# Performance work log

Hardware: AMD Instinct MI355X
Metric: run time of the kernel (lower is better)

The kernel has to match this reference:

```python
import jax, jax.numpy as jnp
import numpy as np

NU, NI, G, D, HD, OD = 8000, 10000, 4096, 64, 64, 64
ALPHA = 0.8      # self vs neighbor mixing in NodeApplyModule
EPS = 1e-8       # cosine-similarity denominator epsilon
NEG_BIG = -1e38  # replacement for all -inf rows


def setup_inputs() -> dict:
    key = jax.random.key(0)
    ks = jax.random.split(key, 24)
    def lin(k, o, i):
        return (jax.random.normal(k, (o, i), jnp.float32) * 0.02)
    def bias(k, o):
        return (jax.random.normal(k, (o,), jnp.float32) * 0.02)
    inp = {}
    inp["H"] = jax.random.randint(ks[0], (NU + NI, G), 0, 2, jnp.int32)
    inp["feats_weight"] = jax.random.normal(ks[1], (NU + NI, D), jnp.float32) * 0.1
    inp["num_groups"] = G
    # user SelfAttention params
    inp["u_Wq"] = lin(ks[2], HD, D); inp["u_bq"] = bias(ks[3], HD)
    inp["u_Wk"] = lin(ks[4], HD, D); inp["u_bk"] = bias(ks[5], HD)
    inp["u_Wv"] = lin(ks[6], HD, D); inp["u_bv"] = bias(ks[7], HD)
    inp["u_Ws"] = lin(ks[8], 1, NU); inp["u_bs"] = bias(ks[9], 1)
    # item SelfAttention params
    inp["i_Wq"] = lin(ks[10], HD, D); inp["i_bq"] = bias(ks[11], HD)
    inp["i_Wk"] = lin(ks[12], HD, D); inp["i_bk"] = bias(ks[13], HD)
    inp["i_Wv"] = lin(ks[14], HD, D); inp["i_bv"] = bias(ks[15], HD)
    inp["i_Ws"] = lin(ks[16], 1, NI); inp["i_bs"] = bias(ks[17], 1)
    # WeightedGCN NodeApplyModule linear: in_feats = 2*HD -> out_feats = OD
    inp["g_W"] = lin(ks[18], OD, 2 * HD); inp["g_b"] = bias(ks[19], OD)
    return inp


def _self_attention(x, mask, num_groups, Wq, bq, Wk, bk, Wv, bv, Ws, bs):
    # x: [N, D] ; mask: [N, G]
    q = x @ Wq.T + bq            # [N, HD]
    k = x @ Wk.T + bk            # [N, HD]
    v = x @ Wv.T + bv            # [N, HD]
    s = (q @ k.T) @ Ws.T + bs    # [N, 1]  (Linear(num_elem,1) over q@k.T)
    scores = jnp.broadcast_to(s.reshape(1, -1), (num_groups, x.shape[0]))  # [G, N]
    maskT = (mask == 0).T        # [G, N]
    scores = jnp.where(maskT, -jnp.inf, scores)
    all_inf = jnp.all(scores == -jnp.inf, axis=1, keepdims=True)
    scores = jnp.where(all_inf, jnp.float32(NEG_BIG), scores)
    w = jax.nn.softmax(scores, axis=1)   # [G, N]
    return w @ v, w                      # [G, HD], [G, N]


def reference(H, feats_weight, num_groups,
              u_Wq, u_bq, u_Wk, u_bk, u_Wv, u_bv, u_Ws, u_bs,
              i_Wq, i_bq, i_Wk, i_bk, i_Wv, i_bv, i_Ws, i_bs,
              g_W, g_b):
    users_feats = feats_weight[:NU]
    items_feats = feats_weight[NU:]
    users_mask = H[:NU]
    items_mask = H[NU:]

    gf_u, w_u = _self_attention(users_feats, users_mask, num_groups,
                                u_Wq, u_bq, u_Wk, u_bk, u_Wv, u_bv, u_Ws, u_bs)
    gf_i, w_i = _self_attention(items_feats, items_mask, num_groups,
                                i_Wq, i_bq, i_Wk, i_bk, i_Wv, i_bv, i_Ws, i_bs)
    # NaN scrubbing (faithful to torch.where(isnan, 0, .))
    gf_i = jnp.where(jnp.isnan(gf_i), 0.0, gf_i)
    w_i = jnp.where(jnp.isnan(w_i), 0.0, w_i)

    group_weights = jnp.concatenate([w_u, w_i], axis=1)   # [G, NU+NI]
    group_feats = jnp.concatenate([gf_u, gf_i], axis=1)   # [G, 2*HD]

    # similarity graph (cosine similarity of group weight rows)
    wp = group_weights @ group_weights.T                  # [G, G]
    norms = jnp.sqrt(jnp.sum(group_weights * group_weights, axis=1))
    l2 = 1.0 / (norms[:, None] * norms[None, :] + EPS)
    A = wp * l2  # edge weight src->dst at A[src, dst]; zero WP entries contribute 0

    # weighted mean aggregation (DGL msg/reduce: sum(w*h)/sum(w) over in-edges)
    msg = A.T @ group_feats                 # [G, 2*HD]: sum_src A[src,dst]*h[src]
    deg = jnp.sum(A, axis=0)[:, None]       # [G, 1]:   sum_src A[src,dst]
    h_neigh = jnp.where(deg > 0, msg / jnp.where(deg > 0, deg, 1.0), 0.0)

    agg = ALPHA * group_feats + (1.0 - ALPHA) * h_neigh
    out = jax.nn.sigmoid(agg @ g_W.T + g_b)               # [G, OD]
    return out
```

## Files before the change

### kernel.cpp

```cpp
#include <hip/hip_runtime.h>
#include <hip/hip_bf16.h>
#include <cstdint>
#include <cstddef>

#define NU   8000
#define NI   10000
#define NTOT 18000
#define G    4096
#define KP2  18176
#define NSL  284
#define NSL128 142
#define KT8  142
#define UT8  63

typedef __attribute__((ext_vector_type(4))) float f32x4;

__device__ __forceinline__ float bfu(unsigned short u){
  return __uint_as_float(((unsigned)u)<<16);
}
__device__ __forceinline__ unsigned short f2b(float f){
  __hip_bfloat16 h = __float2bfloat16(f);
  return __builtin_bit_cast(unsigned short, h);
}
__device__ __forceinline__ unsigned char f2f8(float v){
  int p = __builtin_amdgcn_cvt_pk_fp8_f32(v, 0.f, 0, false);
  return (unsigned char)(p & 0xff);
}
template<int SEL>
__device__ __forceinline__ float f8tof(unsigned int w){
  return __builtin_amdgcn_cvt_f32_fp8((int)w, SEL);
}
__device__ __forceinline__ void async16(void* lds, const void* g){
  __builtin_amdgcn_global_load_lds((const __attribute__((address_space(1))) unsigned int*)g,
                                   (__attribute__((address_space(3))) unsigned int*)lds, 16, 0, 0);
}
__device__ __forceinline__ int slot2n(int s){
  return (s < 8064) ? (s < 8000 ? s : -1) : (s-64 < NTOT ? s-64 : -1);
}

__global__ __launch_bounds__(256) void k_proj(
    const float* __restrict__ feats,
    const float* uWq, const float* ubq, const float* uWk, const float* ubk,
    const float* uWv, const float* ubv, const float* uWs,
    const float* iWq, const float* ibq, const float* iWk, const float* ibk,
    const float* iWv, const float* ibv, const float* iWs,
    float* __restrict__ q, unsigned short* __restrict__ vrow, float* __restrict__ wsk)
{
  __shared__ unsigned short Wt[6*4096];
  __shared__ float bl[6*64];
  __shared__ float wacc[128];
  const float* mats[6]  = {uWq,uWk,uWv,iWq,iWk,iWv};
  const float* bias6[6] = {ubq,ubk,ubv,ibq,ibk,ibv};
  int t = threadIdx.x;
  for (int m=0;m<6;m++)
    for (int e=t; e<4096; e+=256){
      int dd = e>>6, jj = e&63;
      Wt[m*4096 + jj*64 + dd] = f2b(mats[m][e]);
    }
  for (int e=t; e<384; e+=256) bl[e] = bias6[e>>6][e&63];
  if (t<128) wacc[t]=0.f;
  __syncthreads();
  int wave=t>>6, lane=t&63;
  int gw = blockIdx.x*4+wave, nw = gridDim.x*4;
  float accU=0.f, accI=0.f;
  for (int n=gw; n<NTOT; n+=nw){
    int br = (n>=NU);
    const unsigned short* W = Wt + br*3*4096;
    const float* bb = bl + br*192;
    float x = feats[(size_t)n*64+lane];
    float qd=bb[lane], kd=bb[64+lane], vd=bb[128+lane];
    #pragma unroll 16
    for (int j=0;j<64;j++){
      float xj = __shfl(x, j, 64);
      qd += xj * bfu(W[       j*64+lane]);
      kd += xj * bfu(W[4096 + j*64+lane]);
      vd += xj * bfu(W[8192 + j*64+lane]);
    }
    q[(size_t)n*64+lane] = qd;
    vrow[(size_t)n*64+lane] = f2b(vd);
    float wsn = br ? iWs[n-NU] : uWs[n];
    if (br) accI += wsn*kd; else accU += wsn*kd;
  }
  atomicAdd(&wacc[lane], accU);
  atomicAdd(&wacc[64+lane], accI);
  __syncthreads();
  if (t<128) atomicAdd(&wsk[t], wacc[t]);
}

__global__ __launch_bounds__(256) void k_score(const float* __restrict__ q, const float* __restrict__ wsk,
    const float* ubs, const float* ibs, float* __restrict__ rfs, unsigned char* __restrict__ rbs)
{
  __shared__ float wl[128];
  int t=threadIdx.x;
  if (t<128) wl[t]=wsk[t];
  __syncthreads();
  int slot = blockIdx.x*256+t;
  if (slot>=KP2) return;
  int n = slot2n(slot);
  if (n<0){ rfs[slot]=0.f; rbs[slot]=0; return; }
  int br = (slot>=8064);
  const float* wk = wl + br*64;
  float s = br ? ibs[0] : ubs[0];
  const float* qr = q + (size_t)n*64;
  #pragma unroll
  for (int d=0;d<64;d++) s += qr[d]*wk[d];
  unsigned char b = f2f8(expf(s));
  rbs[slot] = b;
  rfs[slot] = f8tof<0>((unsigned int)b);
}

__global__ __launch_bounds__(256) void k_buildW(
    const int* __restrict__ H, const float* __restrict__ rfs, const unsigned char* __restrict__ rbs,
    unsigned char* __restrict__ W8, unsigned char* __restrict__ W8t,
    float* __restrict__ Zu, float* __restrict__ Zi,
    float* __restrict__ S2u, float* __restrict__ S2i)
{
  __shared__ unsigned char Tb[128*136];
  __shared__ float rl[128];
  __shared__ unsigned char rb[128];
  __shared__ float zp[8][128];
  __shared__ float sp[8][128];
  int t = threadIdx.x;
  int s0 = blockIdx.x*128;
  int g0 = blockIdx.y*128;
  int isItem = (s0 >= 8064);
  if (t < 128){
    int n = slot2n(s0+t);
    rl[t] = (n>=0) ? rfs[s0+t] : 0.f;
    rb[t] = (n>=0) ? rbs[s0+t] : (unsigned char)0;
  }
  __syncthreads();
  int rgrp = t>>5;
  int gq   = (t&31)*4;
  int cc   = gq>>4;
  int gi4  = gq&15;
  float za[4]={0.f,0.f,0.f,0.f}, sa[4]={0.f,0.f,0.f,0.f};
  #pragma unroll
  for (int i=0;i<16;i++){
    int row = i*8 + rgrp;
    int n = slot2n(s0+row);
    uchar4 pk; pk.x=0; pk.y=0; pk.z=0; pk.w=0;
    if (n >= 0){
      int4 hv = *(const int4*)(H + (size_t)n*G + g0 + gq);
      unsigned char rbv = rb[row];
      float rq = rl[row];
      if (hv.x){ pk.x=rbv; za[0]+=rq; sa[0]+=rq*rq; }
      if (hv.y){ pk.y=rbv; za[1]+=rq; sa[1]+=rq*rq; }
      if (hv.z){ pk.z=rbv; za[2]+=rq; sa[2]+=rq*rq; }
      if (hv.w){ pk.w=rbv; za[3]+=rq; sa[3]+=rq*rq; }
    }
    int scc = cc ^ ((row>>3)&7);
    *(uchar4*)(Tb + row*136 + (scc<<4) + gi4) = pk;
  }
  #pragma unroll
  for (int e=0;e<4;e++){ zp[rgrp][gq+e]=za[e]; sp[rgrp][gq+e]=sa[e]; }
  __syncthreads();
  #pragma unroll
  for (int p=0;p<4;p++){
    int row = p*32 + (t>>3);
    int c   = t&7;
    int scc = c ^ ((row>>3)&7);
    uint4 v = *(const uint4*)(Tb + row*136 + (scc<<4));
    *(uint4*)(W8t + (size_t)(s0+row)*G + g0 + (c<<4)) = v;
  }
  #pragma unroll
  for (int p=0;p<4;p++){
    int gl = p*32 + (t>>3);
    int sc = (t&7)*16;
    int gcc = gl>>4, gb = gl&15;
    __align__(16) unsigned char buf[16];
    #pragma unroll
    for (int j=0;j<16;j++){
      int row = sc+j;
      int scc = gcc ^ ((row>>3)&7);
      buf[j] = Tb[row*136 + (scc<<4) + gb];
    }
    *(uint4*)(W8 + (size_t)(g0+gl)*KP2 + s0 + sc) = *(uint4*)buf;
  }
  if (t < 128){
    float z=0.f, s2=0.f;
    #pragma unroll
    for (int j=0;j<8;j++){ z += zp[j][t]; s2 += sp[j][t]; }
    if (isItem){ atomicAdd(&Zi[g0+t], z); atomicAdd(&S2i[g0+t], s2); }
    else       { atomicAdd(&Zu[g0+t], z); atomicAdd(&S2u[g0+t], s2); }
  }
}

__global__ __launch_bounds__(256) void k_mid(
    const float* __restrict__ Zu, const float* __restrict__ Zi,
    const float* __restrict__ S2u, const float* __restrict__ S2i,
    float* __restrict__ Cu, float* __restrict__ Ci,
    float* __restrict__ cnu, float* __restrict__ cni, float* __restrict__ ninv,
    unsigned char* __restrict__ W8, unsigned char* __restrict__ W8t,
    const unsigned short* __restrict__ vrow, unsigned char* __restrict__ vt8)
{
  __shared__ unsigned short tile[64][65];
  int b = blockIdx.x;
  int t = threadIdx.x;
  if (b == 0){
    for (int g=t; g<G; g+=256){
      float zu=Zu[g], zi=Zi[g];
      int fu = !(zu>0.f), fi = !(zi>0.f);
      float cu = fu ? (1.f/(float)NU) : 1.f/zu;
      float ci = fi ? (1.f/(float)NI) : 1.f/zi;
      float nu  = fu ? (1.f/(float)NU) : S2u[g]*cu*cu;
      float ni_ = fi ? (1.f/(float)NI) : S2i[g]*ci*ci;
      float nv = rsqrtf(nu+ni_);
      Cu[g]=cu; Ci[g]=ci; ninv[g]=nv; cnu[g]=cu*nv; cni[g]=ci*nv;
      if (fu){ for (int k=0;k<NU;k++){ W8[(size_t)g*KP2+k]=0x38; W8t[(size_t)k*G+g]=0x38; } }
      if (fi){ for (int k=0;k<NI;k++){ W8[(size_t)g*KP2+8064+k]=0x38; W8t[(size_t)(8064+k)*G+g]=0x38; } }
    }
    return;
  }
  int s0 = (b-1)*64;
  int tc = t&63, tr = t>>6;
  #pragma unroll
  for (int i=0;i<16;i++){
    int row = tr+i*4;
    int n = slot2n(s0+row);
    tile[row][tc] = (n>=0) ? vrow[(size_t)n*64+tc] : (unsigned short)0;
  }
  __syncthreads();
  int dOff = (s0 >= 8064) ? 64 : 0;
  #pragma unroll
  for (int i=0;i<16;i++){
    int dd = tr+i*4;
    float v = bfu(tile[tc][dd]) * 16.f;
    vt8[(size_t)(dOff+dd)*KP2 + s0+tc] = f2f8(v);
  }
}

template<int MODE>
__global__ __launch_bounds__(256) void k_gemm(
    const unsigned char* __restrict__ A, const unsigned char* __restrict__ B,
    float* __restrict__ Cs, float* __restrict__ degsl,
    const unsigned char* __restrict__ u8,
    long ldA, long ldB, long ldc)
{
  __shared__ __align__(16) unsigned char As[128*128];
  __shared__ __align__(16) unsigned char Bs[128*128];
  int t=threadIdx.x, wave=t>>6, lane=t&63;
  int I=blockIdx.x, J=blockIdx.y, z=blockIdx.z;
  int kt0=0, ktn=0;
  if (MODE==0){ kt0 = z*9; ktn = min(9, KT8-kt0); }
  else if (MODE==1){ kt0 = z*8; ktn = 8; }
  else {
    if (z<8){ kt0 = z*8;             ktn = min(8,  UT8-kt0); }
    else    { kt0 = UT8 + (z-8)*10;  ktn = min(10, KT8-kt0); }
  }
  f32x4 acc[4][4];
  #pragma unroll
  for (int mi=0;mi<4;mi++)
    #pragma unroll
    for (int ni=0;ni<4;ni++){
      acc[mi][ni][0]=0.f; acc[mi][ni][1]=0.f; acc[mi][ni][2]=0.f; acc[mi][ni][3]=0.f;
    }
  f32x4 accd[4];
  if (MODE==2){
    #pragma unroll
    for (int mi=0;mi<4;mi++){ accd[mi][0]=0.f; accd[mi][1]=0.f; accd[mi][2]=0.f; accd[mi][3]=0.f; }
  }
  int l7 = lane&7, q4 = lane>>4, cl15 = lane&15;
  int rowOff = wave*8 + (lane>>3);
  int cchunk = (lane&7) ^ ((lane>>3)&7);
  long aRow0 = (MODE==1) ? ((J>=UT8)?128:0) : (long)I*128;
  const unsigned char* Abase = A + aRow0*ldA + (long)cchunk*16;
  const unsigned char* Bbase = B + (long)J*128*ldB + (long)cchunk*16;
  unsigned char* AsW = As + wave*1024;
  unsigned char* BsW = Bs + wave*1024;
  int mrow0 = (wave&1)*64, nrow0 = (wave>>1)*64;
  for (int kt=kt0; kt<kt0+ktn; ++kt){
    long k0 = (long)kt*128;
    #pragma unroll
    for (int rr=0; rr<4; rr++){
      async16(AsW + rr*4096, Abase + (long)(rr*32 + rowOff)*ldA + k0);
      async16(BsW + rr*4096, Bbase + (long)(rr*32 + rowOff)*ldB + k0);
    }
    __syncthreads();
    #pragma unroll
    for (int kk=0; kk<4; kk++){
      int xoff = (((kk*2 + (q4>>1)) ^ l7) << 4) + ((q4&1)<<3);
      long af[4], bf[4];
      #pragma unroll
      for (int mi=0;mi<4;mi++)
        af[mi] = *(const long*)(As + (mrow0 + mi*16 + cl15)*128 + xoff);
      #pragma unroll
      for (int ni=0;ni<4;ni++)
        bf[ni] = *(const long*)(Bs + (nrow0 + ni*16 + cl15)*128 + xoff);
      #pragma unroll
      for (int mi=0;mi<4;mi++)
        #pragma unroll
        for (int ni=0;ni<4;ni++)
          acc[mi][ni] = __builtin_amdgcn_mfma_f32_16x16x32_fp8_fp8(af[mi], bf[ni], acc[mi][ni], 0,0,0);
      if (MODE==2){
        long bu = 0;
        if (cl15==0) bu = *(const long*)(u8 + (size_t)kt*128 + kk*32 + q4*8);
        #pragma unroll
        for (int mi=0;mi<4;mi++)
          accd[mi] = __builtin_amdgcn_mfma_f32_16x16x32_fp8_fp8(af[mi], bu, accd[mi], 0,0,0);
      }
    }
    __syncthreads();
  }
  int cq = lane>>4, cl = lane&15;
  float* slice = (MODE==1) ? (Cs + (size_t)z*128*KP2) : (Cs + (size_t)z*G*128);
  #pragma unroll
  for (int mi=0;mi<4;mi++)
    #pragma unroll
    for (int ni=0;ni<4;ni++)
      #pragma unroll
      for (int rg=0;rg<4;rg++){
        int gi = (MODE==1 ? 0 : I*128) + mrow0 + mi*16 + cq*4 + rg;
        int hi = J*128 + nrow0 + ni*16 + cl;
        slice[(size_t)gi*ldc + hi] = acc[mi][ni][rg];
      }
  if (MODE==2 && (wave>>1)==0 && cl15==0){
    #pragma unroll
    for (int mi=0;mi<4;mi++)
      #pragma unroll
      for (int rg=0;rg<4;rg++){
        int gi = I*128 + mrow0 + mi*16 + cq*4 + rg;
        degsl[(size_t)z*G + gi] = accd[mi][rg];
      }
  }
}

__global__ __launch_bounds__(256) void k_red0(const float* __restrict__ gfsl,
    const float* __restrict__ Cu, const float* __restrict__ Ci, float* __restrict__ gf){
  int idx = blockIdx.x*256 + threadIdx.x;
  int gi = idx>>5;
  int hc = (idx&31)*4;
  size_t off = (size_t)gi*128 + hc;
  f32x4 s = {0.f,0.f,0.f,0.f};
  #pragma unroll
  for (int z=0;z<16;z++){
    f32x4 v = *(const f32x4*)(gfsl + (size_t)z*G*128 + off);
    s[0]+=v[0]; s[1]+=v[1]; s[2]+=v[2]; s[3]+=v[3];
  }
  float sc = ((hc&64) ? Ci[gi] : Cu[gi]) * 0.0625f;
  f32x4 r = {s[0]*sc, s[1]*sc, s[2]*sc, s[3]*sc};
  *(f32x4*)(gf + off) = r;
}

__global__ __launch_bounds__(256) void k_red1(const float* __restrict__ tmpsl,
    unsigned char* __restrict__ tmpT8){
  int idx = blockIdx.x*256 + threadIdx.x;
  int d = idx / 4544;
  int n = (idx - d*4544)*4;
  size_t off = (size_t)d*KP2 + n;
  f32x4 s = {0.f,0.f,0.f,0.f};
  #pragma unroll
  for (int z=0;z<4;z++){
    f32x4 v = *(const f32x4*)(tmpsl + (size_t)z*128*KP2 + off);
    s[0]+=v[0]; s[1]+=v[1]; s[2]+=v[2]; s[3]+=v[3];
  }
  uchar4 pk;
  pk.x = f2f8(s[0]); pk.y = f2f8(s[1]); pk.z = f2f8(s[2]); pk.w = f2f8(s[3]);
  *(uchar4*)(tmpT8 + off) = pk;
}

__global__ __launch_bounds__(256) void k_red2(const float* __restrict__ msgsl,
    const float* __restrict__ cnu, const float* __restrict__ cni, float* __restrict__ msg){
  int idx = blockIdx.x*256 + threadIdx.x;
  int gi = idx>>5;
  int hc = (idx&31)*4;
  size_t off = (size_t)gi*128 + hc;
  f32x4 su = {0.f,0.f,0.f,0.f}, si = {0.f,0.f,0.f,0.f};
  #pragma unroll
  for (int z=0;z<8;z++){
    f32x4 v = *(const f32x4*)(msgsl + (size_t)z*G*128 + off);
    su[0]+=v[0]; su[1]+=v[1]; su[2]+=v[2]; su[3]+=v[3];
  }
  #pragma unroll
  for (int z=8;z<16;z++){
    f32x4 v = *(const f32x4*)(msgsl + (size_t)z*G*128 + off);
    si[0]+=v[0]; si[1]+=v[1]; si[2]+=v[2]; si[3]+=v[3];
  }
  float a = cnu[gi]*0.015625f, b = cni[gi]*0.015625f;
  f32x4 r = {su[0]*a+si[0]*b, su[1]*a+si[1]*b, su[2]*a+si[2]*b, su[3]*a+si[3]*b};
  *(f32x4*)(msg + off) = r;
}

__global__ __launch_bounds__(256) void k_buildGfsT2(const float* __restrict__ gf, const float* __restrict__ ninv,
    const float* __restrict__ Cu, const float* __restrict__ Ci, unsigned char* __restrict__ gfsT2_8){
  __shared__ float tile[64][65];
  int g0 = blockIdx.x*64, d0 = blockIdx.y*64;
  int tc=threadIdx.x&63, tr=threadIdx.x>>6;
  #pragma unroll
  for (int i=0;i<16;i++){
    int rr=tr+i*4;
    tile[rr][tc] = gf[(size_t)(g0+rr)*128 + d0+tc] * ninv[g0+rr];
  }
  __syncthreads();
  #pragma unroll
  for (int i=0;i<16;i++){
    int dd=tr+i*4;
    float v = tile[tc][dd] * 64.f;
    int g = g0+tc;
    gfsT2_8[(size_t)(d0+dd)*G + g]     = f2f8(v*Cu[g]);
    gfsT2_8[(size_t)(128+d0+dd)*G + g] = f2f8(v*Ci[g]);
  }
}

__global__ __launch_bounds__(256) void k_u(const unsigned char* __restrict__ W8,
    const float* __restrict__ cnu, const float* __restrict__ cni, float* __restrict__ u){
  long k0 = ((long)blockIdx.x*256 + threadIdx.x)*8;
  if (k0 >= KP2) return;
  int g0 = blockIdx.y*512;
  const float* cn = (k0 < 8064) ? cnu : cni;
  float a[8];
  #pragma unroll
  for (int e=0;e<8;e++) a[e]=0.f;
  for (int j=0;j<512;j++){
    float c = cn[g0+j];
    long w = *(const long*)(W8 + (size_t)(g0+j)*KP2 + k0);
    unsigned int lo = (unsigned int)w, hi = (unsigned int)((unsigned long)w>>32);
    a[0] += f8tof<0>(lo)*c; a[1] += f8tof<1>(lo)*c; a[2] += f8tof<2>(lo)*c; a[3] += f8tof<3>(lo)*c;
    a[4] += f8tof<0>(hi)*c; a[5] += f8tof<1>(hi)*c; a[6] += f8tof<2>(hi)*c; a[7] += f8tof<3>(hi)*c;
  }
  #pragma unroll
  for (int e=0;e<8;e++) atomicAdd(&u[k0+e], a[e]);
}

__global__ void k_u8(const float* __restrict__ u, unsigned char* __restrict__ u8){
  int k = blockIdx.x*256+threadIdx.x;
  if (k<KP2) u8[k] = f2f8(u[k]);
}

__global__ __launch_bounds__(256) void k_final(const float* __restrict__ gf, const float* __restrict__ msg,
    const float* __restrict__ degsl, const float* __restrict__ cnu, const float* __restrict__ cni,
    const float* __restrict__ gW, const float* __restrict__ gb, float* __restrict__ out)
{
  __shared__ float Wl[64*129];
  __shared__ float aggL[4][128];
  __shared__ float gbL[64];
  __shared__ float degL[4];
  int t=threadIdx.x;
  for (int e=t; e<8192; e+=256){ int o=e>>7, dd=e&127; Wl[o*129+dd] = gW[e]; }
  if (t<64) gbL[t] = gb[t];
  int g0 = blockIdx.x*4;
  if (t<4){
    int g = g0+t;
    float su=0.f, si=0.f;
    #pragma unroll
    for (int z=0;z<8;z++)  su += degsl[(size_t)z*G + g];
    #pragma unroll
    for (int z=8;z<16;z++) si += degsl[(size_t)z*G + g];
    degL[t] = cnu[g]*su + cni[g]*si;
  }
  __syncthreads();
  for (int e=t; e<512; e+=256){
    int gl=e>>7, dd=e&127; int g=g0+gl;
    float dv = degL[gl];
    float hn = dv>0.f ? msg[(size_t)g*128+dd]/dv : 0.f;
    aggL[gl][dd] = 0.8f*gf[(size_t)g*128+dd] + 0.2f*hn;
  }
  __syncthreads();
  int gl = t>>6, o = t&63;
  float s = gbL[o];
  #pragma unroll
  for (int dd=0; dd<128; dd++) s += aggL[gl][dd]*Wl[o*129+dd];
  out[(size_t)(g0+gl)*64 + o] = 1.f/(1.f+expf(-s));
}

extern "C" void kernel_launch(void* const* d_in, const int* in_sizes, int n_in,
                              void* d_out, int out_size, void* d_ws, size_t ws_size,
                              hipStream_t stream)
{
  (void)in_sizes; (void)n_in; (void)out_size; (void)ws_size;
  const int* H = (const int*)d_in[0];
  const float* feats = (const float*)d_in[1];
  const float* uWq=(const float*)d_in[3];
  const float* ubq=(const float*)d_in[4];
  const float* uWk=(const float*)d_in[5];
  const float* ubk=(const float*)d_in[6];
  const float* uWv=(const float*)d_in[7];
  const float* ubv=(const float*)d_in[8];
  const float* uWs=(const float*)d_in[9];
  const float* ubs=(const float*)d_in[10];
  const float* iWq=(const float*)d_in[11];
  const float* ibq=(const float*)d_in[12];
  const float* iWk=(const float*)d_in[13];
  const float* ibk=(const float*)d_in[14];
  const float* iWv=(const float*)d_in[15];
  const float* ibv=(const float*)d_in[16];
  const float* iWs=(const float*)d_in[17];
  const float* ibs=(const float*)d_in[18];
  const float* gW =(const float*)d_in[19];
  const float* gb =(const float*)d_in[20];
  float* out = (float*)d_out;

  char* p = (char*)d_ws;
  auto alloc=[&](size_t b)->void*{ void* r=(void*)p; p += (b+255)&~(size_t)255; return r; };
  char* zbase = p;
  float* wsk  = (float*)alloc(128*4);
  float* Zu   = (float*)alloc(G*4);
  float* Zi   = (float*)alloc(G*4);
  float* S2u  = (float*)alloc(G*4);
  float* S2i  = (float*)alloc(G*4);
  float* u    = (float*)alloc((size_t)KP2*4);
  unsigned char* vt8 = (unsigned char*)alloc((size_t)128*KP2);
  size_t zlen = (size_t)(p - zbase);
  unsigned char* W8    = (unsigned char*)alloc((size_t)G*KP2);
  unsigned char* W8t   = (unsigned char*)alloc((size_t)KP2*G);
  unsigned char* tmpT8 = (unsigned char*)alloc((size_t)128*KP2);
  unsigned char* gfsT2_8=(unsigned char*)alloc((size_t)256*G);
  float* gfsl = (float*)alloc((size_t)16*G*128*4);
  float* msgsl= (float*)alloc((size_t)16*G*128*4);
  float* tmpsl= (float*)alloc((size_t)4*128*KP2*4);
  float* degsl= (float*)alloc((size_t)16*G*4);
  float* gf   = (float*)alloc((size_t)G*128*4);
  float* msg  = (float*)alloc((size_t)G*128*4);
  float* q    = (float*)alloc((size_t)NTOT*64*4);
  unsigned short* vrow=(unsigned short*)alloc((size_t)NTOT*64*2);
  float* rfs  = (float*)alloc((size_t)KP2*4);
  unsigned char* rbs = (unsigned char*)alloc((size_t)KP2);
  float* Cu   = (float*)alloc(G*4);
  float* Ci   = (float*)alloc(G*4);
  float* cnu  = (float*)alloc(G*4);
  float* cni  = (float*)alloc(G*4);
  float* ninv = (float*)alloc(G*4);
  unsigned char* u8 = (unsigned char*)alloc((size_t)KP2);

  (void)hipMemsetAsync(zbase, 0, zlen, stream);

  k_proj<<<128,256,0,stream>>>(feats, uWq,ubq,uWk,ubk,uWv,ubv,uWs,
                               iWq,ibq,iWk,ibk,iWv,ibv,iWs, q, vrow, wsk);
  k_score<<<(KP2+255)/256,256,0,stream>>>(q, wsk, ubs, ibs, rfs, rbs);
  k_buildW<<<dim3(NSL128,32),256,0,stream>>>(H, rfs, rbs, W8, W8t, Zu, Zi, S2u, S2i);
  k_mid<<<NSL+1,256,0,stream>>>(Zu,Zi,S2u,S2i,Cu,Ci,cnu,cni,ninv,W8,W8t,vrow,vt8);
  k_gemm<0><<<dim3(32,1,16),256,0,stream>>>(W8, vt8, gfsl, nullptr, nullptr,
                                            (long)KP2, (long)KP2, 128);
  k_red0<<<512,256,0,stream>>>(gfsl, Cu, Ci, gf);
  k_buildGfsT2<<<dim3(64,2),256,0,stream>>>(gf, ninv, Cu, Ci, gfsT2_8);
  k_gemm<1><<<dim3(1,KT8,4),256,0,stream>>>(gfsT2_8, W8t, tmpsl, nullptr, nullptr,
                                            (long)G, (long)G, (long)KP2);
  k_red1<<<2272,256,0,stream>>>(tmpsl, tmpT8);
  k_u<<<dim3(9,8),256,0,stream>>>(W8, cnu, cni, u);
  k_u8<<<(KP2+255)/256,256,0,stream>>>(u, u8);
  k_gemm<2><<<dim3(32,1,16),256,0,stream>>>(W8, tmpT8, msgsl, degsl, u8,
                                            (long)KP2, (long)KP2, 128);
  k_red2<<<512,256,0,stream>>>(msgsl, cnu, cni, msg);
  k_final<<<G/4,256,0,stream>>>(gf, msg, degsl, cnu, cni, gW, gb, out);
}
```

Baseline: 771.5 us.

## Fold u-vector into gemm1 MFMA, fuse reductions, halve split-K slices

Computes the u vector (column weighted sums of W) as an extra fp8 MFMA row inside the second GEMM using fp8-quantized cn scales, removing the separate k_u/k_u8 kernels and their atomics. Fuses the gf slice reduction with the transposed fp8 gfsT2 build into one kernel and merges u8 conversion into k_red1. Split-K depth is doubled, halving partial-slice buffers and reduction traffic but reducing grid parallelism. Quantizing cn to fp8 adds precision risk to u.

```diff
diff --git a/kernel.cpp b/kernel.cpp
--- a/kernel.cpp
+++ b/kernel.cpp
@@ -191,6 +191,7 @@
     const float* __restrict__ S2u, const float* __restrict__ S2i,
     float* __restrict__ Cu, float* __restrict__ Ci,
     float* __restrict__ cnu, float* __restrict__ cni, float* __restrict__ ninv,
+    unsigned char* __restrict__ cn8u, unsigned char* __restrict__ cn8i,
     unsigned char* __restrict__ W8, unsigned char* __restrict__ W8t,
     const unsigned short* __restrict__ vrow, unsigned char* __restrict__ vt8)
 {
@@ -207,6 +208,8 @@
       float ni_ = fi ? (1.f/(float)NI) : S2i[g]*ci*ci;
       float nv = rsqrtf(nu+ni_);
       Cu[g]=cu; Ci[g]=ci; ninv[g]=nv; cnu[g]=cu*nv; cni[g]=ci*nv;
+      cn8u[g] = f2f8(cu*nv*64.f);
+      cn8i[g] = f2f8(ci*nv*64.f);
       if (fu){ for (int k=0;k<NU;k++){ W8[(size_t)g*KP2+k]=0x38; W8t[(size_t)k*G+g]=0x38; } }
       if (fi){ for (int k=0;k<NI;k++){ W8[(size_t)g*KP2+8064+k]=0x38; W8t[(size_t)(8064+k)*G+g]=0x38; } }
     }
@@ -235,6 +238,8 @@
     const unsigned char* __restrict__ A, const unsigned char* __restrict__ B,
     float* __restrict__ Cs, float* __restrict__ degsl,
     const unsigned char* __restrict__ u8,
+    const unsigned char* __restrict__ cn8u, const unsigned char* __restrict__ cn8i,
+    float* __restrict__ uslice,
     long ldA, long ldB, long ldc)
 {
   __shared__ __align__(16) unsigned char As[128*128];
@@ -242,11 +247,11 @@
   int t=threadIdx.x, wave=t>>6, lane=t&63;
   int I=blockIdx.x, J=blockIdx.y, z=blockIdx.z;
   int kt0=0, ktn=0;
-  if (MODE==0){ kt0 = z*9; ktn = min(9, KT8-kt0); }
-  else if (MODE==1){ kt0 = z*8; ktn = 8; }
+  if (MODE==0){ kt0 = z*18; ktn = min(18, KT8-kt0); }
+  else if (MODE==1){ kt0 = z*16; ktn = 16; }
   else {
-    if (z<8){ kt0 = z*8;             ktn = min(8,  UT8-kt0); }
-    else    { kt0 = UT8 + (z-8)*10;  ktn = min(10, KT8-kt0); }
+    if (z<4){ kt0 = z*16;            ktn = min(16, UT8-kt0); }
+    else    { kt0 = UT8 + (z-4)*20;  ktn = min(20, KT8-kt0); }
   }
   f32x4 acc[4][4];
   #pragma unroll
@@ -259,6 +264,11 @@
   if (MODE==2){
     #pragma unroll
     for (int mi=0;mi<4;mi++){ accd[mi][0]=0.f; accd[mi][1]=0.f; accd[mi][2]=0.f; accd[mi][3]=0.f; }
+  }
+  f32x4 accu[4];
+  if (MODE==1){
+    #pragma unroll
+    for (int ni=0;ni<4;ni++){ accu[ni][0]=0.f; accu[ni][1]=0.f; accu[ni][2]=0.f; accu[ni][3]=0.f; }
   }
   int l7 = lane&7, q4 = lane>>4, cl15 = lane&15;
   int rowOff = wave*8 + (lane>>3);
@@ -266,6 +276,7 @@
   long aRow0 = (MODE==1) ? ((J>=UT8)?128:0) : (long)I*128;
   const unsigned char* Abase = A + aRow0*ldA + (long)cchunk*16;
   const unsigned char* Bbase = B + (long)J*128*ldB + (long)cchunk*16;
+  const unsigned char* cnrow = (MODE==1) ? ((J>=UT8) ? cn8i : cn8u) : nullptr;
   unsigned char* AsW = As + wave*1024;
   unsigned char* BsW = Bs + wave*1024;
   int mrow0 = (wave&1)*64, nrow0 = (wave>>1)*64;
@@ -299,6 +310,13 @@
         for (int mi=0;mi<4;mi++)
           accd[mi] = __builtin_amdgcn_mfma_f32_16x16x32_fp8_fp8(af[mi], bu, accd[mi], 0,0,0);
       }
+      if (MODE==1){
+        long au = 0;
+        if (cl15==0) au = *(const long*)(cnrow + (size_t)kt*128 + kk*32 + q4*8);
+        #pragma unroll
+        for (int ni=0;ni<4;ni++)
+          accu[ni] = __builtin_amdgcn_mfma_f32_16x16x32_fp8_fp8(au, bf[ni], accu[ni], 0,0,0);
+      }
     }
     __syncthreads();
   }
@@ -323,39 +341,71 @@
         degsl[(size_t)z*G + gi] = accd[mi][rg];
       }
   }
-}
-
-__global__ __launch_bounds__(256) void k_red0(const float* __restrict__ gfsl,
-    const float* __restrict__ Cu, const float* __restrict__ Ci, float* __restrict__ gf){
-  int idx = blockIdx.x*256 + threadIdx.x;
-  int gi = idx>>5;
-  int hc = (idx&31)*4;
-  size_t off = (size_t)gi*128 + hc;
-  f32x4 s = {0.f,0.f,0.f,0.f};
-  #pragma unroll
-  for (int z=0;z<16;z++){
-    f32x4 v = *(const f32x4*)(gfsl + (size_t)z*G*128 + off);
-    s[0]+=v[0]; s[1]+=v[1]; s[2]+=v[2]; s[3]+=v[3];
-  }
-  float sc = ((hc&64) ? Ci[gi] : Cu[gi]) * 0.0625f;
-  f32x4 r = {s[0]*sc, s[1]*sc, s[2]*sc, s[3]*sc};
-  *(f32x4*)(gf + off) = r;
+  if (MODE==1 && (wave&1)==0 && q4==0){
+    #pragma unroll
+    for (int ni=0;ni<4;ni++){
+      int si = J*128 + nrow0 + ni*16 + cl15;
+      uslice[(size_t)z*KP2 + si] = accu[ni][0];
+    }
+  }
+}
+
+__global__ __launch_bounds__(256) void k_gfpost(const float* __restrict__ gfsl,
+    const float* __restrict__ Cu, const float* __restrict__ Ci, const float* __restrict__ ninv,
+    float* __restrict__ gf, unsigned char* __restrict__ gfsT2_8)
+{
+  __shared__ float tile[64][65];
+  int g0 = blockIdx.x*64, d0 = blockIdx.y*64;
+  int tc=threadIdx.x&63, tr=threadIdx.x>>6;
+  const float* Cd = blockIdx.y ? Ci : Cu;
+  #pragma unroll
+  for (int i=0;i<16;i++){
+    int rr=tr+i*4;
+    size_t off = (size_t)(g0+rr)*128 + d0+tc;
+    float s = 0.f;
+    #pragma unroll
+    for (int zz=0;zz<8;zz++) s += gfsl[(size_t)zz*G*128 + off];
+    float gfv = s * Cd[g0+rr] * 0.0625f;
+    gf[off] = gfv;
+    tile[rr][tc] = gfv * ninv[g0+rr];
+  }
+  __syncthreads();
+  #pragma unroll
+  for (int i=0;i<16;i++){
+    int dd=tr+i*4;
+    float v = tile[tc][dd] * 64.f;
+    int g = g0+tc;
+    gfsT2_8[(size_t)(d0+dd)*G + g]     = f2f8(v*Cu[g]);
+    gfsT2_8[(size_t)(128+d0+dd)*G + g] = f2f8(v*Ci[g]);
+  }
 }
 
 __global__ __launch_bounds__(256) void k_red1(const float* __restrict__ tmpsl,
-    unsigned char* __restrict__ tmpT8){
-  int idx = blockIdx.x*256 + threadIdx.x;
+    unsigned char* __restrict__ tmpT8, const float* __restrict__ uslice, unsigned char* __restrict__ u8){
+  int b = blockIdx.x, t = threadIdx.x;
+  if (b >= 2272){
+    int idx2 = (b-2272)*256 + t;
+    if (idx2 < KP2/4){
+      size_t off = (size_t)idx2*4;
+      f32x4 s = *(const f32x4*)(uslice + off);
+      f32x4 s2 = *(const f32x4*)(uslice + (size_t)KP2 + off);
+      uchar4 pk;
+      pk.x = f2f8((s[0]+s2[0])*0.015625f);
+      pk.y = f2f8((s[1]+s2[1])*0.015625f);
+      pk.z = f2f8((s[2]+s2[2])*0.015625f);
+      pk.w = f2f8((s[3]+s2[3])*0.015625f);
+      *(uchar4*)(u8 + off) = pk;
+    }
+    return;
+  }
+  int idx = b*256 + t;
   int d = idx / 4544;
   int n = (idx - d*4544)*4;
   size_t off = (size_t)d*KP2 + n;
-  f32x4 s = {0.f,0.f,0.f,0.f};
-  #pragma unroll
-  for (int z=0;z<4;z++){
-    f32x4 v = *(const f32x4*)(tmpsl + (size_t)z*128*KP2 + off);
-    s[0]+=v[0]; s[1]+=v[1]; s[2]+=v[2]; s[3]+=v[3];
-  }
+  f32x4 a = *(const f32x4*)(tmpsl + off);
+  f32x4 c = *(const f32x4*)(tmpsl + (size_t)128*KP2 + off);
   uchar4 pk;
-  pk.x = f2f8(s[0]); pk.y = f2f8(s[1]); pk.z = f2f8(s[2]); pk.w = f2f8(s[3]);
+  pk.x = f2f8(a[0]+c[0]); pk.y = f2f8(a[1]+c[1]); pk.z = f2f8(a[2]+c[2]); pk.w = f2f8(a[3]+c[3]);
   *(uchar4*)(tmpT8 + off) = pk;
 }
 
@@ -367,64 +417,18 @@
   size_t off = (size_t)gi*128 + hc;
   f32x4 su = {0.f,0.f,0.f,0.f}, si = {0.f,0.f,0.f,0.f};
   #pragma unroll
-  for (int z=0;z<8;z++){
+  for (int z=0;z<4;z++){
     f32x4 v = *(const f32x4*)(msgsl + (size_t)z*G*128 + off);
     su[0]+=v[0]; su[1]+=v[1]; su[2]+=v[2]; su[3]+=v[3];
   }
   #pragma unroll
-  for (int z=8;z<16;z++){
+  for (int z=4;z<8;z++){
     f32x4 v = *(const f32x4*)(msgsl + (size_t)z*G*128 + off);
     si[0]+=v[0]; si[1]+=v[1]; si[2]+=v[2]; si[3]+=v[3];
   }
   float a = cnu[gi]*0.015625f, b = cni[gi]*0.015625f;
   f32x4 r = {su[0]*a+si[0]*b, su[1]*a+si[1]*b, su[2]*a+si[2]*b, su[3]*a+si[3]*b};
   *(f32x4*)(msg + off) = r;
-}
-
-__global__ __launch_bounds__(256) void k_buildGfsT2(const float* __restrict__ gf, const float* __restrict__ ninv,
-    const float* __restrict__ Cu, const float* __restrict__ Ci, unsigned char* __restrict__ gfsT2_8){
-  __shared__ float tile[64][65];
-  int g0 = blockIdx.x*64, d0 = blockIdx.y*64;
-  int tc=threadIdx.x&63, tr=threadIdx.x>>6;
-  #pragma unroll
-  for (int i=0;i<16;i++){
-    int rr=tr+i*4;
-    tile[rr][tc] = gf[(size_t)(g0+rr)*128 + d0+tc] * ninv[g0+rr];
-  }
-  __syncthreads();
-  #pragma unroll
-  for (int i=0;i<16;i++){
-    int dd=tr+i*4;
-    float v = tile[tc][dd] * 64.f;
-    int g = g0+tc;
-    gfsT2_8[(size_t)(d0+dd)*G + g]     = f2f8(v*Cu[g]);
-    gfsT2_8[(size_t)(128+d0+dd)*G + g] = f2f8(v*Ci[g]);
-  }
-}
-
-__global__ __launch_bounds__(256) void k_u(const unsigned char* __restrict__ W8,
-    const float* __restrict__ cnu, const float* __restrict__ cni, float* __restrict__ u){
-  long k0 = ((long)blockIdx.x*256 + threadIdx.x)*8;
-  if (k0 >= KP2) return;
-  int g0 = blockIdx.y*512;
-  const float* cn = (k0 < 8064) ? cnu : cni;
-  float a[8];
-  #pragma unroll
-  for (int e=0;e<8;e++) a[e]=0.f;
-  for (int j=0;j<512;j++){
-    float c = cn[g0+j];
-    long w = *(const long*)(W8 + (size_t)(g0+j)*KP2 + k0);
-    unsigned int lo = (unsigned int)w, hi = (unsigned int)((unsigned long)w>>32);
-    a[0] += f8tof<0>(lo)*c; a[1] += f8tof<1>(lo)*c; a[2] += f8tof<2>(lo)*c; a[3] += f8tof<3>(lo)*c;
-    a[4] += f8tof<0>(hi)*c; a[5] += f8tof<1>(hi)*c; a[6] += f8tof<2>(hi)*c; a[7] += f8tof<3>(hi)*c;
-  }
-  #pragma unroll
-  for (int e=0;e<8;e++) atomicAdd(&u[k0+e], a[e]);
-}
-
-__global__ void k_u8(const float* __restrict__ u, unsigned char* __restrict__ u8){
-  int k = blockIdx.x*256+threadIdx.x;
-  if (k<KP2) u8[k] = f2f8(u[k]);
 }
 
 __global__ __launch_bounds__(256) void k_final(const float* __restrict__ gf, const float* __restrict__ msg,
@@ -443,9 +447,9 @@
     int g = g0+t;
     float su=0.f, si=0.f;
     #pragma unroll
-    for (int z=0;z<8;z++)  su += degsl[(size_t)z*G + g];
-    #pragma unroll
-    for (int z=8;z<16;z++) si += degsl[(size_t)z*G + g];
+    for (int z=0;z<4;z++) su += degsl[(size_t)z*G + g];
+    #pragma unroll
+    for (int z=4;z<8;z++) si += degsl[(size_t)z*G + g];
     degL[t] = cnu[g]*su + cni[g]*si;
   }
   __syncthreads();
@@ -498,17 +502,17 @@
   float* Zi   = (float*)alloc(G*4);
   float* S2u  = (float*)alloc(G*4);
   float* S2i  = (float*)alloc(G*4);
-  float* u    = (float*)alloc((size_t)KP2*4);
   unsigned char* vt8 = (unsigned char*)alloc((size_t)128*KP2);
   size_t zlen = (size_t)(p - zbase);
   unsigned char* W8    = (unsigned char*)alloc((size_t)G*KP2);
   unsigned char* W8t   = (unsigned char*)alloc((size_t)KP2*G);
   unsigned char* tmpT8 = (unsigned char*)alloc((size_t)128*KP2);
   unsigned char* gfsT2_8=(unsigned char*)alloc((size_t)256*G);
-  float* gfsl = (float*)alloc((size_t)16*G*128*4);
-  float* msgsl= (float*)alloc((size_t)16*G*128*4);
-  float* tmpsl= (float*)alloc((size_t)4*128*KP2*4);
-  float* degsl= (float*)alloc((size_t)16*G*4);
+  float* gfsl = (float*)alloc((size_t)8*G*128*4);
+  float* msgsl= (float*)alloc((size_t)8*G*128*4);
+  float* tmpsl= (float*)alloc((size_t)2*128*KP2*4);
+  float* uslice=(float*)alloc((size_t)2*KP2*4);
+  float* degsl= (float*)alloc((size_t)8*G*4);
   float* gf   = (float*)alloc((size_t)G*128*4);
   float* msg  = (float*)alloc((size_t)G*128*4);
   float* q    = (float*)alloc((size_t)NTOT*64*4);
@@ -520,6 +524,8 @@
   float* cnu  = (float*)alloc(G*4);
   float* cni  = (float*)alloc(G*4);
   float* ninv = (float*)alloc(G*4);
+  unsigned char* cn8u = (unsigned char*)alloc(G);
+  unsigned char* cn8i = (unsigned char*)alloc(G);
   unsigned char* u8 = (unsigned char*)alloc((size_t)KP2);
 
   (void)hipMemsetAsync(zbase, 0, zlen, stream);
@@ -528,18 +534,15 @@
                                iWq,ibq,iWk,ibk,iWv,ibv,iWs, q, vrow, wsk);
   k_score<<<(KP2+255)/256,256,0,stream>>>(q, wsk, ubs, ibs, rfs, rbs);
   k_buildW<<<dim3(NSL128,32),256,0,stream>>>(H, rfs, rbs, W8, W8t, Zu, Zi, S2u, S2i);
-  k_mid<<<NSL+1,256,0,stream>>>(Zu,Zi,S2u,S2i,Cu,Ci,cnu,cni,ninv,W8,W8t,vrow,vt8);
-  k_gemm<0><<<dim3(32,1,16),256,0,stream>>>(W8, vt8, gfsl, nullptr, nullptr,
-                                            (long)KP2, (long)KP2, 128);
-  k_red0<<<512,256,0,stream>>>(gfsl, Cu, Ci, gf);
-  k_buildGfsT2<<<dim3(64,2),256,0,stream>>>(gf, ninv, Cu, Ci, gfsT2_8);
-  k_gemm<1><<<dim3(1,KT8,4),256,0,stream>>>(gfsT2_8, W8t, tmpsl, nullptr, nullptr,
+  k_mid<<<NSL+1,256,0,stream>>>(Zu,Zi,S2u,S2i,Cu,Ci,cnu,cni,ninv,cn8u,cn8i,W8,W8t,vrow,vt8);
+  k_gemm<0><<<dim3(32,1,8),256,0,stream>>>(W8, vt8, gfsl, nullptr, nullptr, nullptr, nullptr, nullptr,
+                                           (long)KP2, (long)KP2, 128);
+  k_gfpost<<<dim3(64,2),256,0,stream>>>(gfsl, Cu, Ci, ninv, gf, gfsT2_8);
+  k_gemm<1><<<dim3(1,KT8,2),256,0,stream>>>(gfsT2_8, W8t, tmpsl, nullptr, nullptr, cn8u, cn8i, uslice,
                                             (long)G, (long)G, (long)KP2);
-  k_red1<<<2272,256,0,stream>>>(tmpsl, tmpT8);
-  k_u<<<dim3(9,8),256,0,stream>>>(W8, cnu, cni, u);
-  k_u8<<<(KP2+255)/256,256,0,stream>>>(u, u8);
-  k_gemm<2><<<dim3(32,1,16),256,0,stream>>>(W8, tmpT8, msgsl, degsl, u8,
-                                            (long)KP2, (long)KP2, 128);
+  k_red1<<<2272+18,256,0,stream>>>(tmpsl, tmpT8, uslice, u8);
+  k_gemm<2><<<dim3(32,1,8),256,0,stream>>>(W8, tmpT8, msgsl, degsl, u8, nullptr, nullptr, nullptr,
+                                           (long)KP2, (long)KP2, 128);
   k_red2<<<512,256,0,stream>>>(msgsl, cnu, cni, msg);
   k_final<<<G/4,256,0,stream>>>(gf, msg, degsl, cnu, cni, gW, gb, out);
 }
```

After: 745.1 us. 1.04x faster.
